# Kernel optimization log

Hardware: AMD Instinct MI355X
Metric: run time of the kernel (lower is better)

Reference implementation:

```python
import jax, jax.numpy as jnp
import numpy as np

K = 20      # kNN neighbors
H = 4       # attention heads
EPS = 1e-5  # BatchNorm eps
NEG = 0.2   # LeakyReLU negative slope


def lrelu(x):
    return jnp.where(x >= 0, x, NEG * x)


def bn(x, g, b):
    # eval-mode BatchNorm: running_mean=0, running_var=1
    return x * (g / jnp.sqrt(1.0 + EPS)) + b


def knn_idx(x):
    # x: (B, N, C) -> (B, N, K) indices of K nearest neighbors (incl. self)
    inner = -2.0 * jnp.einsum('bnc,bmc->bnm', x, x)
    xx = jnp.sum(x * x, axis=-1)
    pd = -xx[:, :, None] - inner - xx[:, None, :]  # negative squared distance
    return jax.lax.top_k(pd, K)[1]


def edge_conv(x, w, g, b):
    # EdgeConv: gather kNN features, cat(nbr-ctr, ctr), 1x1 conv, BN, LeakyReLU, max over K
    idx = knn_idx(x)                                   # (B,N,K)
    nbr = jax.vmap(lambda f, i: f[i])(x, idx)          # (B,N,K,C)
    ctr = jnp.broadcast_to(x[:, :, None, :], nbr.shape)
    e = jnp.concatenate([nbr - ctr, ctr], axis=-1)     # (B,N,K,2C)
    h = lrelu(bn(jnp.einsum('bnkc,oc->bnko', e, w), g, b))
    return jnp.max(h, axis=2)                          # (B,N,Cout)


def mha(x, w_in, b_in, w_out, b_out):
    # Faithful to source: (B,N,E) fed to nn.MultiheadAttention with batch_first=False,
    # so seq length L=B and batch=N (attention mixes across the batch axis).
    L, Nb, E = x.shape
    d = E // H
    qkv = x @ w_in.T + b_in
    q, k, v = jnp.split(qkv, 3, axis=-1)
    q = q.reshape(L, Nb, H, d) * (1.0 / np.sqrt(d))
    k = k.reshape(L, Nb, H, d)
    v = v.reshape(L, Nb, H, d)
    a = jax.nn.softmax(jnp.einsum('lnhd,mnhd->nhlm', q, k), axis=-1)
    o = jnp.einsum('nhlm,mnhd->lnhd', a, v).reshape(L, Nb, E)
    return o @ w_out.T + b_out


def setup_inputs():
    ks = iter(jax.random.split(jax.random.key(0), 64))
    def rn(shape, s=0.05):
        return jax.random.normal(next(ks), shape, jnp.float32) * s
    def gamma(c):
        return 1.0 + rn((c,), 0.1)
    B, N = 8, 1024
    inp = {'x': rn((B, N, 3), 1.0)}
    for i, (ci, co) in enumerate([(6, 64), (128, 64), (128, 128), (256, 256)], 1):
        inp[f'w{i}'] = rn((co, ci)); inp[f'g{i}'] = gamma(co); inp[f'b{i}'] = rn((co,))
    for i, e in enumerate([64, 64, 128, 256], 1):
        inp[f'a{i}_wi'] = rn((3 * e, e)); inp[f'a{i}_bi'] = rn((3 * e,))
        inp[f'a{i}_wo'] = rn((e, e));     inp[f'a{i}_bo'] = rn((e,))
    inp['w5'] = rn((1024, 512)); inp['g5'] = gamma(1024); inp['b5'] = rn((1024,))
    inp['l1w'] = rn((512, 2048)); inp['g6'] = gamma(512); inp['b6'] = rn((512,))
    inp['l2w'] = rn((256, 512)); inp['l2b'] = rn((256,))
    inp['g7'] = gamma(256); inp['b7'] = rn((256,))
    inp['l3w'] = rn((40, 256)); inp['l3b'] = rn((40,))
    return inp


def reference(x, w1, g1, b1, a1_wi, a1_bi, a1_wo, a1_bo,
              w2, g2, b2, a2_wi, a2_bi, a2_wo, a2_bo,
              w3, g3, b3, a3_wi, a3_bi, a3_wo, a3_bo,
              w4, g4, b4, a4_wi, a4_bi, a4_wo, a4_bo,
              w5, g5, b5, l1w, g6, b6, l2w, l2b, g7, b7, l3w, l3b):
    x1 = edge_conv(x, w1, g1, b1)
    x1 = mha(x1, a1_wi, a1_bi, a1_wo, a1_bo) + x1
    x2 = edge_conv(x1, w2, g2, b2)
    x2 = mha(x2, a2_wi, a2_bi, a2_wo, a2_bo) + x2
    x3 = edge_conv(x2, w3, g3, b3)
    x3 = mha(x3, a3_wi, a3_bi, a3_wo, a3_bo) + x3
    x4 = edge_conv(x3, w4, g4, b4)
    x4 = mha(x4, a4_wi, a4_bi, a4_wo, a4_bo) + x4
    h = lrelu(bn(jnp.concatenate([x1, x2, x3, x4], axis=-1) @ w5.T, g5, b5))  # (B,N,1024)
    feat = jnp.concatenate([jnp.max(h, axis=1), jnp.mean(h, axis=1)], axis=-1)  # (B,2048)
    h = lrelu(bn(feat @ l1w.T, g6, b6))
    h = lrelu(bn(h @ l2w.T + l2b, g7, b7))  # dropout is eval-mode identity
    return h @ l3w.T + l3b  # (B, 40)
```

## Files before the change

### kernel.cpp

```cpp
#include <hip/hip_runtime.h>
#include <hip/hip_bf16.h>

#define B_ 8
#define N_ 1024
#define K_ 20
#define BN_ (B_*N_)

#define BN_SCALE 0.9999950000374997f

typedef __attribute__((ext_vector_type(8))) short short8;
typedef __attribute__((ext_vector_type(4))) float f32x4;

__device__ __forceinline__ float US2F(unsigned short u) {
    union { unsigned u; float f; } c; c.u = ((unsigned)u) << 16; return c.f;
}
__device__ __forceinline__ unsigned short F2BF(float f) {
    union { float f; unsigned u; } c; c.f = f;
    unsigned r = c.u + 0x7FFF + ((c.u >> 16) & 1);
    return (unsigned short)(r >> 16);
}

__device__ __forceinline__ void ldsld16(const unsigned short* g, unsigned short* l) {
    __builtin_amdgcn_global_load_lds(
        (const __attribute__((address_space(1))) void*)g,
        (__attribute__((address_space(3))) void*)l, 16, 0, 0);
}

struct DetP { const unsigned short* g[7]; };
__device__ __forceinline__ int det_isbf(const DetP& dp) {
    int cnt = 0;
    #pragma unroll
    for (int i = 0; i < 7; i++) {
        float v = US2F(dp.g[i][0]);
        if (v > 0.5f && v < 1.5f) cnt++;
    }
    return cnt >= 4;
}

struct TPar { const void* src; void* dst; int O, I, blk0, mode; };
struct TList { TPar p[44]; };
struct TrP { const void* src; float* dst; int O, I, bx, blk0; };

__global__ __launch_bounds__(256) void k_prep(TList tl, int nent,
                                              TrP q0, TrP q1, TrP q2,
                                              int nbp, int nbtr,
                                              const void* x0, DetP dp,
                                              unsigned short* __restrict__ xa,
                                              unsigned short* __restrict__ xb,
                                              float* __restrict__ xx1) {
    __shared__ int sbf;
    if (threadIdx.x == 0) sbf = det_isbf(dp);
    __syncthreads();
    const int isbf = sbf;
    auto ld0 = [&](int idx) {
        return isbf ? US2F(((const unsigned short*)x0)[idx])
                    : ((const float*)x0)[idx];
    };
    const int bid = blockIdx.x;
    if (bid >= nbp + nbtr) {
        int blk = bid - nbp - nbtr;
        if (blk >= (BN_ * 32) / 256) {
            int i = (blk - (BN_ * 32) / 256) * 256 + threadIdx.x;
            if (i >= BN_) return;
            float s = 0.f;
            #pragma unroll
            for (int c = 0; c < 3; c++) { float v = ld0(i * 3 + c); s += v * v; }
            xx1[i] = s;
            return;
        }
        const int e = blk * 256 + threadIdx.x;
        const int i = e >> 5, p = e & 31;
        unsigned short va = 0, vb = 0;
        if (p < 9) {
            const int seg = p / 3, c = p - seg * 3;
            const float v = ld0(i * 3 + c);
            const unsigned short h = F2BF(v);
            const unsigned short l = F2BF(v - US2F(h));
            va = (seg == 1) ? l : h;
            vb = (seg < 2) ? h : l;
        }
        xa[e] = va; xb[e] = vb;
        return;
    }
    if (bid >= nbp) {
        int blk = bid - nbp;
        TrP p = q0;
        if (blk >= q2.blk0) p = q2; else if (blk >= q1.blk0) p = q1;
        blk -= p.blk0;
        const int tx = threadIdx.x & 31, ty = threadIdx.x >> 5;
        const int bi = blk % p.bx, bo = blk / p.bx;
        const int i0 = bi * 32, o0 = bo * 32;
        __shared__ float s[32][33];
        #pragma unroll
        for (int r = 0; r < 4; r++) {
            const int o = o0 + ty + r * 8, i = i0 + tx;
            if (o < p.O && i < p.I) {
                const size_t e = (size_t)o * p.I + i;
                s[ty + r * 8][tx] = isbf ? US2F(((const unsigned short*)p.src)[e])
                                         : ((const float*)p.src)[e];
            }
        }
        __syncthreads();
        #pragma unroll
        for (int r = 0; r < 4; r++) {
            const int i = i0 + ty + r * 8, o = o0 + tx;
            if (i < p.I && o < p.O) p.dst[(size_t)i * p.O + o] = s[tx][ty + r * 8];
        }
        return;
    }
    int blk = bid;
    int wi = 0;
    for (int j = nent - 1; j >= 0; j--) { if (blk >= tl.p[j].blk0) { wi = j; break; } }
    const TPar p = tl.p[wi];
    int e = (blk - p.blk0) * 256 + threadIdx.x;
    int n = p.O * p.I;
    if (e >= n) return;
    if (p.mode == 4) { ((float*)p.dst)[e] = 0.f; return; }
    int o = e / p.I, i = e - o * p.I;
    float v = isbf ? US2F(((const unsigned short*)p.src)[e])
                   : ((const float*)p.src)[e];
    if (p.mode == 0) {
        ((float*)p.dst)[(size_t)i * p.O + o] = v;
    } else if (p.mode == 2) {
        ((unsigned short*)p.dst)[e] = F2BF(v);
    } else {
        const int C = p.I >> 1;
        if (i < C) ((unsigned short*)p.dst)[(size_t)o * C + i] = F2BF(v);
        else       ((unsigned short*)p.dst)[(size_t)(p.O + o) * C + (i - C)] = F2BF(v);
    }
}

template<int KP, int TM, int TN>
__global__ __launch_bounds__(256) void k_pdm(const unsigned short* __restrict__ xa,
                                             const unsigned short* __restrict__ xb,
                                             const float* __restrict__ xx,
                                             float* __restrict__ pd) {
    const int bid = blockIdx.x;
    const int b = bid & 7;
    const int tt = bid >> 3;
    const int rb = (tt >> 3) * TM, cb = (tt & 7) * TN;
    const unsigned short* Ab = xa + (size_t)b * N_ * KP;
    const unsigned short* Bb = xb + (size_t)b * N_ * KP;
    const float* xxb = xx + (size_t)b * N_;
    const int t = threadIdx.x;
    __shared__ __align__(16) unsigned short As[2][TM * 32];
    __shared__ __align__(16) unsigned short Bs[2][TN * 32];
    const int w = t >> 6, lane = t & 63;
    constexpr int QR = TM / 2, QC = TN / 2;
    constexpr int MR = QR / 16, NR = QC / 16;
    const int wr = (w & 1) * QR, wc = (w >> 1) * QC;
    const int fr = lane & 15, q = lane >> 4;
    f32x4 acc[MR][NR] = {};

    auto STAGE = [&](int buf, int k0) {
        constexpr int AT = TM * 4;
        #pragma unroll
        for (int R = 0; R < (AT + 255) / 256; R++) {
            const int G = t + R * 256;
            if (AT >= (R + 1) * 256 || G < AT) {
                const int m = G >> 2, gs = (G & 3) ^ ((m >> 1) & 3);
                ldsld16(&Ab[(size_t)(rb + m) * KP + k0 + gs * 8], &As[buf][w * 512 + R * 2048]);
            }
        }
        constexpr int BT = TN * 4;
        #pragma unroll
        for (int R = 0; R < (BT + 255) / 256; R++) {
            const int G = t + R * 256;
            if (BT >= (R + 1) * 256 || G < BT) {
                const int n = G >> 2, gs = (G & 3) ^ ((n >> 1) & 3);
                ldsld16(&Bb[(size_t)(cb + n) * KP + k0 + gs * 8], &Bs[buf][w * 512 + R * 2048]);
            }
        }
    };

    constexpr int NT = KP / 32;
    STAGE(0, 0);
    asm volatile("s_waitcnt vmcnt(0)" ::: "memory");
    __builtin_amdgcn_s_barrier();
    int cur = 0;
    for (int ts = 0; ts < NT; ++ts) {
        if (ts + 1 < NT) STAGE(cur ^ 1, (ts + 1) * 32);
        short8 af[MR], bfr[NR];
        #pragma unroll
        for (int mi = 0; mi < MR; mi++) {
            const int r = wr + mi * 16 + fr;
            af[mi] = *reinterpret_cast<const short8*>(&As[cur][r * 32 + ((q ^ ((r >> 1) & 3)) << 3)]);
        }
        #pragma unroll
        for (int ni = 0; ni < NR; ni++) {
            const int r = wc + ni * 16 + fr;
            bfr[ni] = *reinterpret_cast<const short8*>(&Bs[cur][r * 32 + ((q ^ ((r >> 1) & 3)) << 3)]);
        }
        #pragma unroll
        for (int mi = 0; mi < MR; mi++) {
            #pragma unroll
            for (int ni = 0; ni < NR; ni++)
                acc[mi][ni] = __builtin_amdgcn_mfma_f32_16x16x32_bf16(af[mi], bfr[ni], acc[mi][ni], 0, 0, 0);
        }
        asm volatile("s_waitcnt vmcnt(0)" ::: "memory");
        __builtin_amdgcn_s_barrier();
        cur ^= 1;
    }
    float* pdb = pd + (size_t)b * N_ * N_;
    const int cr = (lane >> 4) * 4, cc = lane & 15;
    #pragma unroll
    for (int mi = 0; mi < MR; mi++) {
        #pragma unroll
        for (int ni = 0; ni < NR; ni++) {
            #pragma unroll
            for (int r = 0; r < 4; r++) {
                const int row = rb + wr + mi * 16 + cr + r;
                const int col = cb + wc + ni * 16 + cc;
                pdb[(size_t)row * N_ + col] = 2.f * acc[mi][ni][r] - xxb[col];
            }
        }
    }
}

__device__ __forceinline__ void sel_dev(const float* __restrict__ pd,
                                        int* __restrict__ idx, int blk) {
    const int w = threadIdx.x >> 6, lane = threadIdx.x & 63;
    const int b = blk & 7;
    const int i = (b << 10) + ((blk >> 3) << 2) + w;
    const float* row = pd + (size_t)b * N_ * N_ + (size_t)(i & 1023) * N_;
    unsigned key[16];
    #pragma unroll
    for (int q = 0; q < 16; q++) {
        const int j = q * 64 + lane;
        unsigned bits = __float_as_uint(row[j]);
        bits = (bits & 0x80000000u) ? ~bits : (bits | 0x80000000u);
        key[q] = (bits & 0xFFFFFC00u) | (unsigned)(N_ - 1 - j);
    }
    int myj = 0;
    for (int kk = 0; kk < K_; kk++) {
        unsigned m = key[0];
        #pragma unroll
        for (int u = 1; u < 16; u++) m = key[u] > m ? key[u] : m;
        #pragma unroll
        for (int s = 1; s < 64; s <<= 1) {
            unsigned o = (unsigned)__shfl_xor((int)m, s, 64);
            m = o > m ? o : m;
        }
        const int j = N_ - 1 - (int)(m & 1023u);
        if (lane == kk) myj = j;
        #pragma unroll
        for (int u = 0; u < 16; u++)
            if (key[u] == m) key[u] = 0u;
    }
    if (lane < K_) idx[(size_t)i * K_ + lane] = myj;
}

template<int KD, int NC, int TM, int TN, bool CATA, bool POOL, int SPLIT>
__device__ __forceinline__ void gemm_dev(int bx, int by,
                                         const unsigned short* __restrict__ A,
                                         const unsigned short* __restrict__ A2,
                                         const unsigned short* __restrict__ A3,
                                         const unsigned short* __restrict__ A4,
                                         const unsigned short* __restrict__ Bw,
                                         const float* __restrict__ bias,
                                         const float* __restrict__ resid,
                                         float* __restrict__ Cout,
                                         float* __restrict__ Cz, int yco,
                                         int scale_cols, float qs,
                                         const float* __restrict__ gamma,
                                         const float* __restrict__ beta,
                                         unsigned short* __restrict__ obf,
                                         unsigned* __restrict__ pmaxu,
                                         float* __restrict__ psum,
                                         unsigned short* __restrict__ sxa,
                                         unsigned short* __restrict__ sxb,
                                         float* __restrict__ xxo) {
    const int t = threadIdx.x;
    const int rb = bx * TM, cb = by * TN;
    const int w = t >> 6, lane = t & 63;
    constexpr int QR = TM / 2, QC = TN / 2;
    constexpr int MR = QR / 16, NR = QC / 16;
    const int wr = (w & 1) * QR, wc = (w >> 1) * QC;
    const int fr = lane & 15, q = lane >> 4, fq = q * 8;
    f32x4 acc[MR][NR] = {};
    if constexpr (KD % 32 == 0) {
        __shared__ __align__(16) unsigned short As[2][TM * 32];
        __shared__ __align__(16) unsigned short Bs[2][TN * 32];
        auto STAGE = [&](int buf, int k0) {
            const unsigned short* Asrc = A; int AC = KD, ac0 = k0;
            if constexpr (CATA) {
                if (k0 >= 256)      { Asrc = A4; AC = 256; ac0 = k0 - 256; }
                else if (k0 >= 128) { Asrc = A3; AC = 128; ac0 = k0 - 128; }
                else if (k0 >= 64)  { Asrc = A2; AC = 64;  ac0 = k0 - 64; }
                else                { Asrc = A;  AC = 64;  ac0 = k0; }
            }
            constexpr int AT = TM * 4;
            #pragma unroll
            for (int R = 0; R < (AT + 255) / 256; R++) {
                const int G = t + R * 256;
                if (AT >= (R + 1) * 256 || G < AT) {
                    const int m = G >> 2, gs = (G & 3) ^ ((m >> 1) & 3);
                    ldsld16(&Asrc[(size_t)(rb + m) * AC + ac0 + gs * 8], &As[buf][w * 512 + R * 2048]);
                }
            }
            constexpr int BT = TN * 4;
            #pragma unroll
            for (int R = 0; R < (BT + 255) / 256; R++) {
                const int G = t + R * 256;
                if (BT >= (R + 1) * 256 || G < BT) {
                    const int n = G >> 2, gs = (G & 3) ^ ((n >> 1) & 3);
                    ldsld16(&Bw[(size_t)(cb + n) * KD + k0 + gs * 8], &Bs[buf][w * 512 + R * 2048]);
                }
            }
        };
        constexpr int NT = KD / 32;
        STAGE(0, 0);
        asm volatile("s_waitcnt vmcnt(0)" ::: "memory");
        __builtin_amdgcn_s_barrier();
        int cur = 0;
        for (int ts = 0; ts < NT; ++ts) {
            if (ts + 1 < NT) STAGE(cur ^ 1, (ts + 1) * 32);
            short8 af[MR], bfr[NR];
            #pragma unroll
            for (int mi = 0; mi < MR; mi++) {
                const int r = wr + mi * 16 + fr;
                af[mi] = *reinterpret_cast<const short8*>(&As[cur][r * 32 + ((q ^ ((r >> 1) & 3)) << 3)]);
            }
            #pragma unroll
            for (int ni = 0; ni < NR; ni++) {
                const int r = wc + ni * 16 + fr;
                bfr[ni] = *reinterpret_cast<const short8*>(&Bs[cur][r * 32 + ((q ^ ((r >> 1) & 3)) << 3)]);
            }
            #pragma unroll
            for (int mi = 0; mi < MR; mi++) {
                #pragma unroll
                for (int ni = 0; ni < NR; ni++)
                    acc[mi][ni] = __builtin_amdgcn_mfma_f32_16x16x32_bf16(af[mi], bfr[ni], acc[mi][ni], 0, 0, 0);
            }
            asm volatile("s_waitcnt vmcnt(0)" ::: "memory");
            __builtin_amdgcn_s_barrier();
            cur ^= 1;
        }
    } else {
        __shared__ __align__(16) unsigned short As[TM * 40];
        __shared__ __align__(16) unsigned short Bs[TN * 40];
        for (int k0 = 0; k0 < KD; k0 += 32) {
            __syncthreads();
            #pragma unroll
            for (int u = t; u < TM * 4; u += 256) {
                const int m = u >> 2, c = (u & 3) * 8;
                #pragma unroll
                for (int j = 0; j < 8; j++) {
                    const int kk = k0 + c + j;
                    As[m * 40 + c + j] = (kk < KD) ? A[(size_t)(rb + m) * KD + kk] : (unsigned short)0;
                }
            }
            #pragma unroll
            for (int u = t; u < TN * 4; u += 256) {
                const int n = u >> 2, c = (u & 3) * 8;
                const int gn = cb + n;
                if (gn < NC) {
                    #pragma unroll
                    for (int j = 0; j < 8; j++) {
                        const int kk = k0 + c + j;
                        Bs[n * 40 + c + j] = (kk < KD) ? Bw[(size_t)gn * KD + kk] : (unsigned short)0;
                    }
                } else {
                    short8 z = {};
                    *reinterpret_cast<short8*>(&Bs[n * 40 + c]) = z;
                }
            }
            __syncthreads();
            short8 af[MR], bfr[NR];
            #pragma unroll
            for (int mi = 0; mi < MR; mi++)
                af[mi] = *reinterpret_cast<const short8*>(&As[(wr + mi * 16 + fr) * 40 + fq]);
            #pragma unroll
            for (int ni = 0; ni < NR; ni++)
                bfr[ni] = *reinterpret_cast<const short8*>(&Bs[(wc + ni * 16 + fr) * 40 + fq]);
            #pragma unroll
            for (int mi = 0; mi < MR; mi++) {
                #pragma unroll
                for (int ni = 0; ni < NR; ni++)
                    acc[mi][ni] = __builtin_amdgcn_mfma_f32_16x16x32_bf16(af[mi], bfr[ni], acc[mi][ni], 0, 0, 0);
            }
        }
    }
    const int cr = (lane >> 4) * 4, cc = lane & 15;
    if constexpr (POOL) {
        const int bidx = rb >> 10;
        #pragma unroll
        for (int ni = 0; ni < NR; ni++) {
            const int col = cb + wc + ni * 16 + cc;
            const float gm = gamma[col] * BN_SCALE, bt = beta[col];
            float sm = 0.f, mxv = -3e38f;
            #pragma unroll
            for (int mi = 0; mi < MR; mi++) {
                #pragma unroll
                for (int r = 0; r < 4; r++) {
                    float v = acc[mi][ni][r] * gm + bt;
                    v = v >= 0.f ? v : 0.2f * v;
                    sm += v; mxv = fmaxf(mxv, v);
                }
            }
            sm += __shfl_xor(sm, 16, 64);
            sm += __shfl_xor(sm, 32, 64);
            mxv = fmaxf(mxv, __shfl_xor(mxv, 16, 64));
            mxv = fmaxf(mxv, __shfl_xor(mxv, 32, 64));
            if (lane < 16) {
                atomicAdd(&psum[bidx * 1024 + col], sm);
                unsigned tb = __float_as_uint(mxv);
                tb = (tb & 0x80000000u) ? ~tb : (tb | 0x80000000u);
                atomicMax(&pmaxu[bidx * 1024 + col], tb);
            }
        }
    } else {
        float sx[MR][4] = {};
        #pragma unroll
        for (int mi = 0; mi < MR; mi++) {
            #pragma unroll
            for (int ni = 0; ni < NR; ni++) {
                #pragma unroll
                for (int r = 0; r < 4; r++) {
                    const int row = rb + wr + mi * 16 + cr + r;
                    const int col = cb + wc + ni * 16 + cc;
                    if (col < NC) {
                        float v = acc[mi][ni][r] + (bias ? bias[col] : 0.f);
                        if (col < scale_cols) v *= qs;
                        if (resid) v += resid[(size_t)row * NC + col];
                        if (gamma) {
                            v = v * (gamma[col] * BN_SCALE) + beta[col];
                            v = v >= 0.f ? v : 0.2f * v;
                        }
                        if (yco > 0) {
                            if (col < yco) Cout[(size_t)row * yco + col] = v;
                            else           Cz[(size_t)row * yco + (col - yco)] = v;
                        } else {
                            Cout[(size_t)row * NC + col] = v;
                        }
                        if (obf) obf[(size_t)row * NC + col] = F2BF(v);
                        if constexpr (SPLIT > 0) {
                            constexpr int KP2 = 3 * SPLIT;
                            const unsigned short h = F2BF(v);
                            const unsigned short l = F2BF(v - US2F(h));
                            sxa[(size_t)row * KP2 + 0 * SPLIT + col] = h;
                            sxa[(size_t)row * KP2 + 1 * SPLIT + col] = l;
                            sxa[(size_t)row * KP2 + 2 * SPLIT + col] = h;
                            sxb[(size_t)row * KP2 + 0 * SPLIT + col] = h;
                            sxb[(size_t)row * KP2 + 1 * SPLIT + col] = h;
                            sxb[(size_t)row * KP2 + 2 * SPLIT + col] = l;
                            sx[mi][r] += v * v;
                        }
                    }
                }
            }
        }
        if constexpr (SPLIT > 0) {
            #pragma unroll
            for (int mi = 0; mi < MR; mi++) {
                #pragma unroll
                for (int r = 0; r < 4; r++) {
                    float s = sx[mi][r];
                    s += __shfl_xor(s, 1, 64);
                    s += __shfl_xor(s, 2, 64);
                    s += __shfl_xor(s, 4, 64);
                    s += __shfl_xor(s, 8, 64);
                    if ((lane & 15) == 0)
                        atomicAdd(&xxo[rb + wr + mi * 16 + cr + r], s);
                }
            }
        }
    }
}

template<int KD, int NC, int TM, int TN, bool CATA = false, bool POOL = false, int SPLIT = 0, bool AFF = false>
__global__ __launch_bounds__(256) void k_gemmb(const unsigned short* __restrict__ A,
                                               const unsigned short* __restrict__ A2,
                                               const unsigned short* __restrict__ A3,
                                               const unsigned short* __restrict__ A4,
                                               const unsigned short* __restrict__ Bw,
                                               const float* __restrict__ bias,
                                               const float* __restrict__ resid,
                                               float* __restrict__ Cout,
                                               int scale_cols, float qs,
                                               const float* __restrict__ gamma,
                                               const float* __restrict__ beta,
                                               unsigned short* __restrict__ obf,
                                               unsigned* __restrict__ pmaxu,
                                               float* __restrict__ psum,
                                               unsigned short* __restrict__ sxa,
                                               unsigned short* __restrict__ sxb,
                                               float* __restrict__ xxo) {
    int bx = blockIdx.x;
    if constexpr (AFF) bx = (bx & 7) * (gridDim.x >> 3) + (bx >> 3);
    gemm_dev<KD, NC, TM, TN, CATA, POOL, SPLIT>(bx, blockIdx.y,
        A, A2, A3, A4, Bw, bias, resid, Cout, nullptr, 0, scale_cols, qs, gamma, beta,
        obf, pmaxu, psum, sxa, sxb, xxo);
}

template<int KD, int NC, int TM, int TN>
__global__ __launch_bounds__(256) void k_selyz(const float* __restrict__ pd,
                                               int* __restrict__ idx, int selb, int gx,
                                               const unsigned short* __restrict__ A,
                                               const unsigned short* __restrict__ Bw,
                                               float* __restrict__ Cy,
                                               float* __restrict__ Cz, int yco) {
    if ((int)blockIdx.x < selb) { sel_dev(pd, idx, blockIdx.x); return; }
    const int g = blockIdx.x - selb;
    const int batch = g & 7, rem = g >> 3;
    const int rpb = gx >> 3;
    const int bx = batch * rpb + rem % rpb;
    const int by = rem / rpb;
    gemm_dev<KD, NC, TM, TN, false, false, 0>(bx, by,
        A, nullptr, nullptr, nullptr, Bw, nullptr, nullptr, Cy, Cz, yco, 0, 1.f,
        nullptr, nullptr, nullptr, nullptr, nullptr, nullptr, nullptr, nullptr);
}

template<int CO>
__global__ __launch_bounds__(256) void k_edgemax(const float* __restrict__ y,
                                                 const float* __restrict__ z,
                                                 const int* __restrict__ idx,
                                                 const float* __restrict__ g,
                                                 const float* __restrict__ bb,
                                                 float* __restrict__ out,
                                                 unsigned short* __restrict__ outb) {
    constexpr int TPP = CO / 4;
    constexpr int PPB = 256 / TPP;
    const int t = threadIdx.x;
    const int p = t / TPP;
    const int cw = (t % TPP) * 4;
    const int batch = blockIdx.x & 7;
    const int within = blockIdx.x >> 3;
    const int i0 = batch * N_ + within * PPB;
    const int bbase = batch << 10;
    __shared__ int sidx[PPB][K_];
    for (int u = t; u < PPB * K_; u += 256) {
        int pp = u / K_, kk = u - pp * K_;
        sidx[pp][kk] = idx[(size_t)(i0 + pp) * K_ + kk];
    }
    __syncthreads();
    const int ig = i0 + p;
    float4 m = {-3e38f, -3e38f, -3e38f, -3e38f};
    #pragma unroll 4
    for (int k = 0; k < K_; k++) {
        const int jg = bbase + sidx[p][k];
        const float4 yv = *reinterpret_cast<const float4*>(&y[(size_t)jg * CO + cw]);
        m.x = fmaxf(m.x, yv.x); m.y = fmaxf(m.y, yv.y);
        m.z = fmaxf(m.z, yv.z); m.w = fmaxf(m.w, yv.w);
    }
    const float4 yi = *reinterpret_cast<const float4*>(&y[(size_t)ig * CO + cw]);
    const float4 zi = *reinterpret_cast<const float4*>(&z[(size_t)ig * CO + cw]);
    const float4 gv = *reinterpret_cast<const float4*>(&g[cw]);
    const float4 bv = *reinterpret_cast<const float4*>(&bb[cw]);
    float vals[4] = {m.x - yi.x + zi.x, m.y - yi.y + zi.y,
                     m.z - yi.z + zi.z, m.w - yi.w + zi.w};
    float gs[4] = {gv.x, gv.y, gv.z, gv.w};
    float bs[4] = {bv.x, bv.y, bv.z, bv.w};
    float4 o;
    float* op = &o.x;
    #pragma unroll
    for (int j = 0; j < 4; j++) {
        float h = vals[j] * (gs[j] * BN_SCALE) + bs[j];
        op[j] = h >= 0.f ? h : 0.2f * h;
    }
    *reinterpret_cast<float4*>(&out[(size_t)ig * CO + cw]) = o;
    #pragma unroll
    for (int j = 0; j < 4; j++) outb[(size_t)ig * CO + cw + j] = F2BF(op[j]);
}

template<int E>
__global__ __launch_bounds__(256) void k_attn(const float* __restrict__ qkv,
                                              unsigned short* __restrict__ o) {
    constexpr int H = 4, D = E / H, L = 8;
    const int n = blockIdx.x;
    const int t = threadIdx.x;
    const int h = t >> 6, lane = t & 63;
    __shared__ float sq[L][3 * E];
    __shared__ float so[L][E];
    for (int u = t; u < L * 3 * E; u += 256) {
        int l = u / (3 * E), r = u - l * (3 * E);
        sq[l][r] = qkv[(size_t)(l * N_ + n) * (3 * E) + r];
    }
    __syncthreads();
    const int l = lane >> 3, m = lane & 7;
    float s = 0.f;
    #pragma unroll 8
    for (int dd = 0; dd < D; dd++)
        s += sq[l][h * D + dd] * sq[m][E + h * D + dd];
    float mx = s;
    #pragma unroll
    for (int st = 1; st < 8; st <<= 1) mx = fmaxf(mx, __shfl_xor(mx, st, 64));
    float e = expf(s - mx);
    float sum = e;
    #pragma unroll
    for (int st = 1; st < 8; st <<= 1) sum += __shfl_xor(sum, st, 64);
    const float p = e / sum;
    float pm[8];
    #pragma unroll
    for (int mm = 0; mm < 8; mm++) pm[mm] = __shfl(p, (lane & 56) | mm, 64);
    #pragma unroll
    for (int j = 0; j < D / 8; j++) {
        const int dd = m + 8 * j;
        float a = 0.f;
        #pragma unroll
        for (int mm = 0; mm < 8; mm++) a += pm[mm] * sq[mm][2 * E + h * D + dd];
        so[l][h * D + dd] = a;
    }
    __syncthreads();
    for (int u = t; u < L * E; u += 256) {
        int l2 = u / E, e2 = u - l2 * E;
        o[(size_t)(l2 * N_ + n) * E + e2] = F2BF(so[l2][e2]);
    }
}

template<int E, int SPLIT>
__global__ __launch_bounds__(256) void k_attnout(const float* __restrict__ qkv,
                                                 const unsigned short* __restrict__ wo,
                                                 const float* __restrict__ bo,
                                                 float* __restrict__ x,
                                                 unsigned short* __restrict__ xob,
                                                 unsigned short* __restrict__ sxa,
                                                 unsigned short* __restrict__ sxb,
                                                 float* __restrict__ xxo) {
    constexpr int H = 4, D = E / H, L = 8;
    const int n = blockIdx.x;
    const int t = threadIdx.x;
    const int h = t >> 6, lane = t & 63;
    __shared__ float sq[L][3 * E];
    __shared__ float so[L][E];
    __shared__ unsigned short swo[E][E + 8];
    __shared__ float sxx[L];
    for (int u = t; u < L * 3 * E; u += 256) {
        int l = u / (3 * E), r = u - l * (3 * E);
        sq[l][r] = qkv[(size_t)(l * N_ + n) * (3 * E) + r];
    }
    for (int u = t; u < E * E; u += 256) swo[u / E][u % E] = wo[u];
    if (t < L) sxx[t] = 0.f;
    __syncthreads();
    const int l = lane >> 3, m = lane & 7;
    float s = 0.f;
    #pragma unroll 8
    for (int dd = 0; dd < D; dd++)
        s += sq[l][h * D + dd] * sq[m][E + h * D + dd];
    float mx = s;
    #pragma unroll
    for (int st = 1; st < 8; st <<= 1) mx = fmaxf(mx, __shfl_xor(mx, st, 64));
    float e = expf(s - mx);
    float sum = e;
    #pragma unroll
    for (int st = 1; st < 8; st <<= 1) sum += __shfl_xor(sum, st, 64);
    const float p = e / sum;
    float pm[8];
    #pragma unroll
    for (int mm = 0; mm < 8; mm++) pm[mm] = __shfl(p, (lane & 56) | mm, 64);
    #pragma unroll
    for (int j = 0; j < D / 8; j++) {
        const int dd = m + 8 * j;
        float a = 0.f;
        #pragma unroll
        for (int mm = 0; mm < 8; mm++) a += pm[mm] * sq[mm][2 * E + h * D + dd];
        so[l][h * D + dd] = a;
    }
    __syncthreads();
    for (int u = t; u < L * E; u += 256)
        so[u / E][u % E] = US2F(F2BF(so[u / E][u % E]));
    __syncthreads();
    constexpr int PT = (L * E) / 256;
    #pragma unroll
    for (int it = 0; it < PT; it++) {
        const int item = t + it * 256;
        const int ll = item / E, ee = item % E;
        float acc = 0.f;
        #pragma unroll 16
        for (int c = 0; c < E; c++)
            acc += so[ll][c] * US2F(swo[ee][c]);
        const int row = ll * N_ + n;
        const float v = acc + bo[ee] + x[(size_t)row * E + ee];
        x[(size_t)row * E + ee] = v;
        xob[(size_t)row * E + ee] = F2BF(v);
        if constexpr (SPLIT > 0) {
            constexpr int KP2 = 3 * SPLIT;
            const unsigned short hh = F2BF(v);
            const unsigned short lo = F2BF(v - US2F(hh));
            sxa[(size_t)row * KP2 + 0 * SPLIT + ee] = hh;
            sxa[(size_t)row * KP2 + 1 * SPLIT + ee] = lo;
            sxa[(size_t)row * KP2 + 2 * SPLIT + ee] = hh;
            sxb[(size_t)row * KP2 + 0 * SPLIT + ee] = hh;
            sxb[(size_t)row * KP2 + 1 * SPLIT + ee] = hh;
            sxb[(size_t)row * KP2 + 2 * SPLIT + ee] = lo;
            float vs = v * v;
            #pragma unroll
            for (int st = 1; st < 64; st <<= 1) vs += __shfl_xor(vs, st, 64);
            if (lane == 0) atomicAdd(&sxx[ll], vs);
        }
    }
    if constexpr (SPLIT > 0) {
        __syncthreads();
        if (t < L) xxo[t * N_ + n] = sxx[t];
    }
}

__global__ __launch_bounds__(256) void k_fc1(const unsigned* __restrict__ pmaxu,
                                             const float* __restrict__ psum,
                                             const float* __restrict__ l1wT,
                                             const float* __restrict__ g6, const float* __restrict__ b6,
                                             float* __restrict__ f1) {
    int oc = blockIdx.x, b = blockIdx.y, t = threadIdx.x;
    __shared__ float fin[2048];
    __shared__ float ps[4][64];
    for (int u = t; u < 2048; u += 256) {
        float v;
        if (u < 1024) {
            unsigned tb = pmaxu[b * 1024 + u];
            unsigned bits = (tb & 0x80000000u) ? (tb & 0x7FFFFFFFu) : ~tb;
            v = __uint_as_float(bits);
        } else {
            v = psum[b * 1024 + (u - 1024)] * (1.f / 1024.f);
        }
        fin[u] = v;
    }
    __syncthreads();
    int ol = t & 63, kc = t >> 6;
    int o = oc * 64 + ol;
    float acc = 0.f;
    for (int c = kc * 512; c < kc * 512 + 512; c++) acc += fin[c] * l1wT[(size_t)c * 512 + o];
    ps[kc][ol] = acc;
    __syncthreads();
    if (t < 64) {
        int oo = oc * 64 + t;
        float a = ps[0][t] + ps[1][t] + ps[2][t] + ps[3][t];
        float h = a * (g6[oo] * BN_SCALE) + b6[oo];
        f1[b * 512 + oo] = h >= 0.f ? h : 0.2f * h;
    }
}

__global__ __launch_bounds__(256) void k_fc23(const float* __restrict__ f1, const float* __restrict__ l2wT,
                                              const float* __restrict__ l2b,
                                              const float* __restrict__ g7, const float* __restrict__ b7,
                                              const float* __restrict__ l3wT, const float* __restrict__ l3b,
                                              void* __restrict__ out, DetP dp) {
    int b = blockIdx.x, t = threadIdx.x;
    __shared__ float fin[512];
    __shared__ float f2s[256];
    __shared__ int sbf;
    if (t == 0) sbf = det_isbf(dp);
    for (int u = t; u < 512; u += 256) fin[u] = f1[b * 512 + u];
    __syncthreads();
    {
        float acc = 0.f;
        for (int c = 0; c < 512; c++) acc += fin[c] * l2wT[(size_t)c * 256 + t];
        acc += l2b[t];
        float h = acc * (g7[t] * BN_SCALE) + b7[t];
        f2s[t] = h >= 0.f ? h : 0.2f * h;
    }
    __syncthreads();
    if (t < 40) {
        float acc = 0.f;
        for (int c = 0; c < 256; c++) acc += f2s[c] * l3wT[(size_t)c * 40 + t];
        acc += l3b[t];
        if (sbf) ((__hip_bfloat16*)out)[b * 40 + t] = __float2bfloat16(acc);
        else     ((float*)out)[b * 40 + t] = acc;
    }
}

extern "C" void kernel_launch(void* const* d_in, const int* in_sizes, int n_in,
                              void* d_out, int out_size, void* d_ws, size_t ws_size,
                              hipStream_t stream) {
    auto us = [&](int i) { return (const unsigned short*)d_in[i]; };

    float* ws = (float*)d_ws;
    size_t off = 0;
    auto A = [&](size_t n) { float* p = ws + off; off += (n + 3) & ~(size_t)3; return p; };
    auto AU = [&](size_t n) { return (unsigned short*)A((n + 1) / 2); };
    float* x1   = A((size_t)BN_ * 64);
    float* x2   = A((size_t)BN_ * 64);
    float* x3   = A((size_t)BN_ * 128);
    float* x4   = A((size_t)BN_ * 256);
    float* pd   = A((size_t)BN_ * 1024);
    float* f1   = A(8 * 512);
    float* xx   = A(4 * BN_);
    int*   idx  = (int*)A((size_t)BN_ * K_);
    float* qkvw = A((size_t)BN_ * 768);
    unsigned short* xa = AU((size_t)BN_ * 384);
    unsigned short* xb = AU((size_t)BN_ * 384);
    unsigned short* xf0b = AU((size_t)BN_ * 3);
    unsigned short* x1b  = AU((size_t)BN_ * 64);
    unsigned short* x2b  = AU((size_t)BN_ * 64);
    unsigned short* x3b  = AU((size_t)BN_ * 128);
    unsigned short* x4b  = AU((size_t)BN_ * 256);
    unsigned short* owb  = AU((size_t)BN_ * 256);
    unsigned* pmaxu = (unsigned*)A(8 * 1024);
    float*    psum  = A(8 * 1024);
    unsigned short* w1yzb = AU(128 * 3);
    unsigned short* w2yzb = AU(128 * 64);
    unsigned short* w3yzb = AU(256 * 64);
    unsigned short* w4yzb = AU(512 * 128);
    unsigned short* a1wib = AU(192 * 64);  unsigned short* a1wob = AU(64 * 64);
    unsigned short* a2wib = AU(192 * 64);  unsigned short* a2wob = AU(64 * 64);
    unsigned short* a3wib = AU(384 * 128); unsigned short* a3wob = AU(128 * 128);
    unsigned short* a4wib = AU(768 * 256); unsigned short* a4wob = AU(256 * 256);
    unsigned short* w5b   = AU(1024 * 512);
    float* l1wT  = A(2048 * 512);
    float* l2wT  = A(512 * 256);
    float* l3wT  = A(256 * 40);
    float* g1f = A(64);   float* b1f = A(64);
    float* g2f = A(64);   float* b2f = A(64);
    float* g3f = A(128);  float* b3f = A(128);
    float* g4f = A(256);  float* b4f = A(256);
    float* bi1 = A(192);  float* bo1 = A(64);
    float* bi2 = A(192);  float* bo2 = A(64);
    float* bi3 = A(384);  float* bo3 = A(128);
    float* bi4 = A(768);  float* bo4 = A(256);
    float* g5f = A(1024); float* b5f = A(1024);
    float* g6f = A(512);  float* b6f = A(512);
    float* l2bf = A(256);
    float* g7f = A(256);  float* b7f = A(256);
    float* l3bf = A(40);

    float* xx1 = xx;              float* xx2 = xx + BN_;
    float* xx3 = xx + 2 * BN_;    float* xx4 = xx + 3 * BN_;

    float* yy = qkvw;
    float* zz = qkvw + (size_t)BN_ * 256;

    DetP dp{{us(2), us(5), us(8), us(11), us(30), us(33), us(37)}};

    TList tl; int nb = 0; int k = 0;
    auto add = [&](int i, void* dst, int O, int I, int mode) {
        tl.p[k].src = d_in[i]; tl.p[k].dst = dst; tl.p[k].O = O; tl.p[k].I = I;
        tl.p[k].blk0 = nb; tl.p[k].mode = mode;
        nb += (O * I + 255) / 256; k++;
    };
    add(0,  xf0b,  BN_ * 3, 1, 2);
    add(0,  pmaxu, 16384, 1, 4);
    add(1,  w1yzb, 64, 6, 3);
    add(4,  w2yzb, 64, 128, 3);
    add(7,  w3yzb, 128, 128, 3);
    add(10, w4yzb, 256, 256, 3);
    add(13, a1wib, 192, 64, 2);
    add(15, a1wob, 64, 64, 2);
    add(17, a2wib, 192, 64, 2);
    add(19, a2wob, 64, 64, 2);
    add(21, a3wib, 384, 128, 2);
    add(23, a3wob, 128, 128, 2);
    add(25, a4wib, 768, 256, 2);
    add(27, a4wob, 256, 256, 2);
    add(29, w5b,   1024, 512, 2);
    add(2,  g1f, 64, 1, 0);   add(3,  b1f, 64, 1, 0);
    add(5,  g2f, 64, 1, 0);   add(6,  b2f, 64, 1, 0);
    add(8,  g3f, 128, 1, 0);  add(9,  b3f, 128, 1, 0);
    add(11, g4f, 256, 1, 0);  add(12, b4f, 256, 1, 0);
    add(14, bi1, 192, 1, 0);  add(16, bo1, 64, 1, 0);
    add(18, bi2, 192, 1, 0);  add(20, bo2, 64, 1, 0);
    add(22, bi3, 384, 1, 0);  add(24, bo3, 128, 1, 0);
    add(26, bi4, 768, 1, 0);  add(28, bo4, 256, 1, 0);
    add(30, g5f, 1024, 1, 0); add(31, b5f, 1024, 1, 0);
    add(33, g6f, 512, 1, 0);  add(34, b6f, 512, 1, 0);
    add(36, l2bf, 256, 1, 0);
    add(37, g7f, 256, 1, 0);  add(38, b7f, 256, 1, 0);
    add(40, l3bf, 40, 1, 0);

    TrP tp1{d_in[32], l1wT, 512, 2048, 2048 / 32, 0};
    TrP tp2{d_in[35], l2wT, 256, 512,  512 / 32,  (2048 / 32) * (512 / 32)};
    TrP tp3{d_in[39], l3wT, 40,  256,  256 / 32,  tp2.blk0 + (512 / 32) * (256 / 32)};
    const int trblocks = tp3.blk0 + (256 / 32) * ((40 + 31) / 32);
    const int splblocks = (BN_ * 32) / 256 + 32;
    k_prep<<<nb + trblocks + splblocks, 256, 0, stream>>>(
        tl, k, tp1, tp2, tp3, nb, trblocks, d_in[0], dp, xa, xb, xx1);

    const unsigned short* N0 = nullptr;
    unsigned short* U0 = nullptr;
    unsigned* NU = nullptr; float* NF = nullptr;

    k_pdm<32, 128, 128><<<512, 256, 0, stream>>>(xa, xb, xx1, pd);
    k_selyz<3, 128, 64, 64><<<2048 + 256, 256, 0, stream>>>(pd, idx, 2048, 128, xf0b, w1yzb, yy, zz, 64);
    k_edgemax<64><<<BN_ / 16, 256, 0, stream>>>(yy, zz, idx, g1f, b1f, x1, x1b);
    k_gemmb<64, 192, 64, 64, false, false, 0, true><<<dim3(128, 3), 256, 0, stream>>>(x1b, N0, N0, N0, a1wib, bi1, nullptr, qkvw, 64, 0.25f, nullptr, nullptr, nullptr, NU, NF, U0, U0, NF);
    k_attnout<64, 64><<<N_, 256, 0, stream>>>(qkvw, a1wob, bo1, x1, x1b, xa, xb, xx2);

    k_pdm<192, 128, 128><<<512, 256, 0, stream>>>(xa, xb, xx2, pd);
    k_selyz<64, 128, 64, 64><<<2048 + 256, 256, 0, stream>>>(pd, idx, 2048, 128, x1b, w2yzb, yy, zz, 64);
    k_edgemax<64><<<BN_ / 16, 256, 0, stream>>>(yy, zz, idx, g2f, b2f, x2, x2b);
    k_gemmb<64, 192, 64, 64, false, false, 0, true><<<dim3(128, 3), 256, 0, stream>>>(x2b, N0, N0, N0, a2wib, bi2, nullptr, qkvw, 64, 0.25f, nullptr, nullptr, nullptr, NU, NF, U0, U0, NF);
    k_attnout<64, 64><<<N_, 256, 0, stream>>>(qkvw, a2wob, bo2, x2, x2b, xa, xb, xx3);

    k_pdm<192, 128, 128><<<512, 256, 0, stream>>>(xa, xb, xx3, pd);
    k_selyz<64, 256, 64, 64><<<2048 + 512, 256, 0, stream>>>(pd, idx, 2048, 128, x2b, w3yzb, yy, zz, 128);
    k_edgemax<128><<<BN_ / 8, 256, 0, stream>>>(yy, zz, idx, g3f, b3f, x3, x3b);
    k_gemmb<128, 384, 64, 128, false, false, 0, true><<<dim3(128, 3), 256, 0, stream>>>(x3b, N0, N0, N0, a3wib, bi3, nullptr, qkvw, 128, 0.17677669529663687f, nullptr, nullptr, nullptr, NU, NF, U0, U0, NF);
    k_attnout<128, 128><<<N_, 256, 0, stream>>>(qkvw, a3wob, bo3, x3, x3b, xa, xb, xx4);

    k_pdm<384, 128, 128><<<512, 256, 0, stream>>>(xa, xb, xx4, pd);
    k_selyz<128, 512, 128, 128><<<2048 + 256, 256, 0, stream>>>(pd, idx, 2048, 64, x3b, w4yzb, yy, zz, 256);
    k_edgemax<256><<<BN_ / 4, 256, 0, stream>>>(yy, zz, idx, g4f, b4f, x4, x4b);
    k_gemmb<256, 768, 64, 128, false, false, 0, true><<<dim3(128, 6), 256, 0, stream>>>(x4b, N0, N0, N0, a4wib, bi4, nullptr, qkvw, 256, 0.125f, nullptr, nullptr, nullptr, NU, NF, U0, U0, NF);
    k_attn<256><<<N_, 256, 0, stream>>>(qkvw, owb);
    k_gemmb<256, 256, 64, 128, false, false, 0, true><<<dim3(128, 2), 256, 0, stream>>>(owb, N0, N0, N0, a4wob, bo4, x4, x4, 0, 1.f, nullptr, nullptr, x4b, NU, NF, U0, U0, NF);

    k_gemmb<512, 1024, 128, 128, true, true, 0, true><<<dim3(64, 8), 256, 0, stream>>>(
        x1b, x2b, x3b, x4b, w5b, nullptr, nullptr, nullptr, 0, 1.f, g5f, b5f, nullptr, pmaxu, psum, U0, U0, NF);
    k_fc1<<<dim3(8, 8), 256, 0, stream>>>(pmaxu, psum, l1wT, g6f, b6f, f1);
    k_fc23<<<8, 256, 0, stream>>>(f1, l2wT, l2bf, g7f, b7f, l3wT, l3bf, d_out, dp);
}
```

Baseline: 486.4 us.

## Re-fuse kNN pipeline stages and merge final attention with output projection

The pairwise-distance GEMM is moved into the same launch as the y/z edge-feature GEMM, and top-k selection is fused with the edge max-gather. This removes the global idx buffer and one kernel launch per EdgeConv layer. For layer 4, the attention kernel and the output-projection GEMM are merged into one per-point kernel that computes the Wo product from shared memory with scalar FMAs, dropping the bf16 intermediate buffer. The trade-offs are less efficient non-MFMA arithmetic for the layer-4 projection, and select blocks in which only some threads do the gather work (for CO=64 only 64 threads).

```diff
diff --git a/kernel.cpp b/kernel.cpp
--- a/kernel.cpp
+++ b/kernel.cpp
@@ -131,11 +131,11 @@
 }
 
 template<int KP, int TM, int TN>
-__global__ __launch_bounds__(256) void k_pdm(const unsigned short* __restrict__ xa,
-                                             const unsigned short* __restrict__ xb,
-                                             const float* __restrict__ xx,
-                                             float* __restrict__ pd) {
-    const int bid = blockIdx.x;
+__device__ __forceinline__ void pdm_dev(int bid,
+                                        const unsigned short* __restrict__ xa,
+                                        const unsigned short* __restrict__ xb,
+                                        const float* __restrict__ xx,
+                                        float* __restrict__ pd) {
     const int b = bid & 7;
     const int tt = bid >> 3;
     const int rb = (tt >> 3) * TM, cb = (tt & 7) * TN;
@@ -215,39 +215,6 @@
             }
         }
     }
-}
-
-__device__ __forceinline__ void sel_dev(const float* __restrict__ pd,
-                                        int* __restrict__ idx, int blk) {
-    const int w = threadIdx.x >> 6, lane = threadIdx.x & 63;
-    const int b = blk & 7;
-    const int i = (b << 10) + ((blk >> 3) << 2) + w;
-    const float* row = pd + (size_t)b * N_ * N_ + (size_t)(i & 1023) * N_;
-    unsigned key[16];
-    #pragma unroll
-    for (int q = 0; q < 16; q++) {
-        const int j = q * 64 + lane;
-        unsigned bits = __float_as_uint(row[j]);
-        bits = (bits & 0x80000000u) ? ~bits : (bits | 0x80000000u);
-        key[q] = (bits & 0xFFFFFC00u) | (unsigned)(N_ - 1 - j);
-    }
-    int myj = 0;
-    for (int kk = 0; kk < K_; kk++) {
-        unsigned m = key[0];
-        #pragma unroll
-        for (int u = 1; u < 16; u++) m = key[u] > m ? key[u] : m;
-        #pragma unroll
-        for (int s = 1; s < 64; s <<= 1) {
-            unsigned o = (unsigned)__shfl_xor((int)m, s, 64);
-            m = o > m ? o : m;
-        }
-        const int j = N_ - 1 - (int)(m & 1023u);
-        if (lane == kk) myj = j;
-        #pragma unroll
-        for (int u = 0; u < 16; u++)
-            if (key[u] == m) key[u] = 0u;
-    }
-    if (lane < K_) idx[(size_t)i * K_ + lane] = myj;
 }
 
 template<int KD, int NC, int TM, int TN, bool CATA, bool POOL, int SPLIT>
@@ -493,118 +460,102 @@
         obf, pmaxu, psum, sxa, sxb, xxo);
 }
 
-template<int KD, int NC, int TM, int TN>
-__global__ __launch_bounds__(256) void k_selyz(const float* __restrict__ pd,
-                                               int* __restrict__ idx, int selb, int gx,
-                                               const unsigned short* __restrict__ A,
-                                               const unsigned short* __restrict__ Bw,
+template<int KP, int KDY, int NCY, int TMY, int TNY>
+__global__ __launch_bounds__(256) void k_pdmyz(const unsigned short* __restrict__ xa,
+                                               const unsigned short* __restrict__ xb,
+                                               const float* __restrict__ xx,
+                                               float* __restrict__ pd,
+                                               const unsigned short* __restrict__ Ay,
+                                               const unsigned short* __restrict__ Bwy,
                                                float* __restrict__ Cy,
-                                               float* __restrict__ Cz, int yco) {
-    if ((int)blockIdx.x < selb) { sel_dev(pd, idx, blockIdx.x); return; }
-    const int g = blockIdx.x - selb;
+                                               float* __restrict__ Cz, int yco, int gxy) {
+    if ((int)blockIdx.x < 512) { pdm_dev<KP, 128, 128>(blockIdx.x, xa, xb, xx, pd); return; }
+    const int g = blockIdx.x - 512;
     const int batch = g & 7, rem = g >> 3;
-    const int rpb = gx >> 3;
+    const int rpb = gxy >> 3;
     const int bx = batch * rpb + rem % rpb;
     const int by = rem / rpb;
-    gemm_dev<KD, NC, TM, TN, false, false, 0>(bx, by,
-        A, nullptr, nullptr, nullptr, Bw, nullptr, nullptr, Cy, Cz, yco, 0, 1.f,
+    gemm_dev<KDY, NCY, TMY, TNY, false, false, 0>(bx, by,
+        Ay, nullptr, nullptr, nullptr, Bwy, nullptr, nullptr, Cy, Cz, yco, 0, 1.f,
         nullptr, nullptr, nullptr, nullptr, nullptr, nullptr, nullptr, nullptr);
 }
 
 template<int CO>
-__global__ __launch_bounds__(256) void k_edgemax(const float* __restrict__ y,
+__global__ __launch_bounds__(256) void k_seledge(const float* __restrict__ pd,
+                                                 const float* __restrict__ y,
                                                  const float* __restrict__ z,
-                                                 const int* __restrict__ idx,
                                                  const float* __restrict__ g,
                                                  const float* __restrict__ bb,
                                                  float* __restrict__ out,
                                                  unsigned short* __restrict__ outb) {
+    const int t = threadIdx.x;
+    const int w = t >> 6, lane = t & 63;
+    const int blk = blockIdx.x;
+    const int b = blk & 7;
+    const int i0 = (b << 10) + ((blk >> 3) << 2);
+    const int bbase = b << 10;
+    __shared__ int sidx[4][K_];
+    {
+        const int i = i0 + w;
+        const float* row = pd + (size_t)b * N_ * N_ + (size_t)(i & 1023) * N_;
+        unsigned key[16];
+        #pragma unroll
+        for (int q = 0; q < 16; q++) {
+            const int j = q * 64 + lane;
+            unsigned bits = __float_as_uint(row[j]);
+            bits = (bits & 0x80000000u) ? ~bits : (bits | 0x80000000u);
+            key[q] = (bits & 0xFFFFFC00u) | (unsigned)(N_ - 1 - j);
+        }
+        int myj = 0;
+        for (int kk = 0; kk < K_; kk++) {
+            unsigned m = key[0];
+            #pragma unroll
+            for (int u = 1; u < 16; u++) m = key[u] > m ? key[u] : m;
+            #pragma unroll
+            for (int s = 1; s < 64; s <<= 1) {
+                unsigned o = (unsigned)__shfl_xor((int)m, s, 64);
+                m = o > m ? o : m;
+            }
+            const int j = N_ - 1 - (int)(m & 1023u);
+            if (lane == kk) myj = j;
+            #pragma unroll
+            for (int u = 0; u < 16; u++)
+                if (key[u] == m) key[u] = 0u;
+        }
+        if (lane < K_) sidx[w][lane] = myj;
+    }
+    __syncthreads();
     constexpr int TPP = CO / 4;
-    constexpr int PPB = 256 / TPP;
-    const int t = threadIdx.x;
-    const int p = t / TPP;
-    const int cw = (t % TPP) * 4;
-    const int batch = blockIdx.x & 7;
-    const int within = blockIdx.x >> 3;
-    const int i0 = batch * N_ + within * PPB;
-    const int bbase = batch << 10;
-    __shared__ int sidx[PPB][K_];
-    for (int u = t; u < PPB * K_; u += 256) {
-        int pp = u / K_, kk = u - pp * K_;
-        sidx[pp][kk] = idx[(size_t)(i0 + pp) * K_ + kk];
-    }
-    __syncthreads();
-    const int ig = i0 + p;
-    float4 m = {-3e38f, -3e38f, -3e38f, -3e38f};
-    #pragma unroll 4
-    for (int k = 0; k < K_; k++) {
-        const int jg = bbase + sidx[p][k];
-        const float4 yv = *reinterpret_cast<const float4*>(&y[(size_t)jg * CO + cw]);
-        m.x = fmaxf(m.x, yv.x); m.y = fmaxf(m.y, yv.y);
-        m.z = fmaxf(m.z, yv.z); m.w = fmaxf(m.w, yv.w);
-    }
-    const float4 yi = *reinterpret_cast<const float4*>(&y[(size_t)ig * CO + cw]);
-    const float4 zi = *reinterpret_cast<const float4*>(&z[(size_t)ig * CO + cw]);
-    const float4 gv = *reinterpret_cast<const float4*>(&g[cw]);
-    const float4 bv = *reinterpret_cast<const float4*>(&bb[cw]);
-    float vals[4] = {m.x - yi.x + zi.x, m.y - yi.y + zi.y,
-                     m.z - yi.z + zi.z, m.w - yi.w + zi.w};
-    float gs[4] = {gv.x, gv.y, gv.z, gv.w};
-    float bs[4] = {bv.x, bv.y, bv.z, bv.w};
-    float4 o;
-    float* op = &o.x;
-    #pragma unroll
-    for (int j = 0; j < 4; j++) {
-        float h = vals[j] * (gs[j] * BN_SCALE) + bs[j];
-        op[j] = h >= 0.f ? h : 0.2f * h;
-    }
-    *reinterpret_cast<float4*>(&out[(size_t)ig * CO + cw]) = o;
-    #pragma unroll
-    for (int j = 0; j < 4; j++) outb[(size_t)ig * CO + cw + j] = F2BF(op[j]);
-}
-
-template<int E>
-__global__ __launch_bounds__(256) void k_attn(const float* __restrict__ qkv,
-                                              unsigned short* __restrict__ o) {
-    constexpr int H = 4, D = E / H, L = 8;
-    const int n = blockIdx.x;
-    const int t = threadIdx.x;
-    const int h = t >> 6, lane = t & 63;
-    __shared__ float sq[L][3 * E];
-    __shared__ float so[L][E];
-    for (int u = t; u < L * 3 * E; u += 256) {
-        int l = u / (3 * E), r = u - l * (3 * E);
-        sq[l][r] = qkv[(size_t)(l * N_ + n) * (3 * E) + r];
-    }
-    __syncthreads();
-    const int l = lane >> 3, m = lane & 7;
-    float s = 0.f;
-    #pragma unroll 8
-    for (int dd = 0; dd < D; dd++)
-        s += sq[l][h * D + dd] * sq[m][E + h * D + dd];
-    float mx = s;
-    #pragma unroll
-    for (int st = 1; st < 8; st <<= 1) mx = fmaxf(mx, __shfl_xor(mx, st, 64));
-    float e = expf(s - mx);
-    float sum = e;
-    #pragma unroll
-    for (int st = 1; st < 8; st <<= 1) sum += __shfl_xor(sum, st, 64);
-    const float p = e / sum;
-    float pm[8];
-    #pragma unroll
-    for (int mm = 0; mm < 8; mm++) pm[mm] = __shfl(p, (lane & 56) | mm, 64);
-    #pragma unroll
-    for (int j = 0; j < D / 8; j++) {
-        const int dd = m + 8 * j;
-        float a = 0.f;
-        #pragma unroll
-        for (int mm = 0; mm < 8; mm++) a += pm[mm] * sq[mm][2 * E + h * D + dd];
-        so[l][h * D + dd] = a;
-    }
-    __syncthreads();
-    for (int u = t; u < L * E; u += 256) {
-        int l2 = u / E, e2 = u - l2 * E;
-        o[(size_t)(l2 * N_ + n) * E + e2] = F2BF(so[l2][e2]);
+    if (t < 4 * TPP) {
+        const int p = t / TPP;
+        const int cw = (t % TPP) * 4;
+        const int ig = i0 + p;
+        float4 m = {-3e38f, -3e38f, -3e38f, -3e38f};
+        #pragma unroll 4
+        for (int k = 0; k < K_; k++) {
+            const int jg = bbase + sidx[p][k];
+            const float4 yv = *reinterpret_cast<const float4*>(&y[(size_t)jg * CO + cw]);
+            m.x = fmaxf(m.x, yv.x); m.y = fmaxf(m.y, yv.y);
+            m.z = fmaxf(m.z, yv.z); m.w = fmaxf(m.w, yv.w);
+        }
+        const float4 yi = *reinterpret_cast<const float4*>(&y[(size_t)ig * CO + cw]);
+        const float4 zi = *reinterpret_cast<const float4*>(&z[(size_t)ig * CO + cw]);
+        const float4 gv = *reinterpret_cast<const float4*>(&g[cw]);
+        const float4 bv = *reinterpret_cast<const float4*>(&bb[cw]);
+        float vals[4] = {m.x - yi.x + zi.x, m.y - yi.y + zi.y,
+                         m.z - yi.z + zi.z, m.w - yi.w + zi.w};
+        float gs[4] = {gv.x, gv.y, gv.z, gv.w};
+        float bs[4] = {bv.x, bv.y, bv.z, bv.w};
+        float4 o;
+        float* op = &o.x;
+        #pragma unroll
+        for (int j = 0; j < 4; j++) {
+            float h = vals[j] * (gs[j] * BN_SCALE) + bs[j];
+            op[j] = h >= 0.f ? h : 0.2f * h;
+        }
+        *reinterpret_cast<float4*>(&out[(size_t)ig * CO + cw]) = o;
+        #pragma unroll
+        for (int j = 0; j < 4; j++) outb[(size_t)ig * CO + cw + j] = F2BF(op[j]);
     }
 }
 
@@ -695,6 +646,81 @@
     }
 }
 
+__global__ __launch_bounds__(256) void k_attnout4(const float* __restrict__ qkv,
+                                                  const unsigned short* __restrict__ wo,
+                                                  const float* __restrict__ bo,
+                                                  float* __restrict__ x,
+                                                  unsigned short* __restrict__ xob) {
+    constexpr int E = 256, H = 4, D = E / H, L = 8;
+    const int n = blockIdx.x;
+    const int t = threadIdx.x;
+    const int h = t >> 6, lane = t & 63;
+    __shared__ float sq[L][3 * E];
+    __shared__ float so[L][E];
+    __shared__ float swoc[E][33];
+    for (int u = t; u < L * 3 * E; u += 256) {
+        int l = u / (3 * E), r = u - l * (3 * E);
+        sq[l][r] = qkv[(size_t)(l * N_ + n) * (3 * E) + r];
+    }
+    __syncthreads();
+    const int l = lane >> 3, m = lane & 7;
+    float s = 0.f;
+    #pragma unroll 8
+    for (int dd = 0; dd < D; dd++)
+        s += sq[l][h * D + dd] * sq[m][E + h * D + dd];
+    float mx = s;
+    #pragma unroll
+    for (int st = 1; st < 8; st <<= 1) mx = fmaxf(mx, __shfl_xor(mx, st, 64));
+    float e = expf(s - mx);
+    float sum = e;
+    #pragma unroll
+    for (int st = 1; st < 8; st <<= 1) sum += __shfl_xor(sum, st, 64);
+    const float p = e / sum;
+    float pm[8];
+    #pragma unroll
+    for (int mm = 0; mm < 8; mm++) pm[mm] = __shfl(p, (lane & 56) | mm, 64);
+    #pragma unroll
+    for (int j = 0; j < D / 8; j++) {
+        const int dd = m + 8 * j;
+        float a = 0.f;
+        #pragma unroll
+        for (int mm = 0; mm < 8; mm++) a += pm[mm] * sq[mm][2 * E + h * D + dd];
+        so[l][h * D + dd] = a;
+    }
+    __syncthreads();
+    for (int u = t; u < L * E; u += 256)
+        so[u / E][u % E] = US2F(F2BF(so[u / E][u % E]));
+    constexpr int PT = (L * E) / 256;
+    float acc[PT] = {};
+    for (int ch = 0; ch < 8; ch++) {
+        __syncthreads();
+        for (int u = t; u < E * 32; u += 256) {
+            const int ee = u >> 5, cc = u & 31;
+            swoc[ee][cc] = US2F(wo[ee * E + ch * 32 + cc]);
+        }
+        __syncthreads();
+        #pragma unroll
+        for (int it = 0; it < PT; it++) {
+            const int item = t + it * 256;
+            const int ll = item / E, ee = item % E;
+            float a = acc[it];
+            #pragma unroll
+            for (int cc = 0; cc < 32; cc++)
+                a += so[ll][ch * 32 + cc] * swoc[ee][cc];
+            acc[it] = a;
+        }
+    }
+    #pragma unroll
+    for (int it = 0; it < PT; it++) {
+        const int item = t + it * 256;
+        const int ll = item / E, ee = item % E;
+        const int row = ll * N_ + n;
+        const float v = acc[it] + bo[ee] + x[(size_t)row * E + ee];
+        x[(size_t)row * E + ee] = v;
+        xob[(size_t)row * E + ee] = F2BF(v);
+    }
+}
+
 __global__ __launch_bounds__(256) void k_fc1(const unsigned* __restrict__ pmaxu,
                                              const float* __restrict__ psum,
                                              const float* __restrict__ l1wT,
@@ -774,7 +800,6 @@
     float* pd   = A((size_t)BN_ * 1024);
     float* f1   = A(8 * 512);
     float* xx   = A(4 * BN_);
-    int*   idx  = (int*)A((size_t)BN_ * K_);
     float* qkvw = A((size_t)BN_ * 768);
     unsigned short* xa = AU((size_t)BN_ * 384);
     unsigned short* xb = AU((size_t)BN_ * 384);
@@ -783,7 +808,6 @@
     unsigned short* x2b  = AU((size_t)BN_ * 64);
     unsigned short* x3b  = AU((size_t)BN_ * 128);
     unsigned short* x4b  = AU((size_t)BN_ * 256);
-    unsigned short* owb  = AU((size_t)BN_ * 256);
     unsigned* pmaxu = (unsigned*)A(8 * 1024);
     float*    psum  = A(8 * 1024);
     unsigned short* w1yzb = AU(128 * 3);
@@ -867,30 +891,25 @@
     unsigned short* U0 = nullptr;
     unsigned* NU = nullptr; float* NF = nullptr;
 
-    k_pdm<32, 128, 128><<<512, 256, 0, stream>>>(xa, xb, xx1, pd);
-    k_selyz<3, 128, 64, 64><<<2048 + 256, 256, 0, stream>>>(pd, idx, 2048, 128, xf0b, w1yzb, yy, zz, 64);
-    k_edgemax<64><<<BN_ / 16, 256, 0, stream>>>(yy, zz, idx, g1f, b1f, x1, x1b);
+    k_pdmyz<32, 3, 128, 64, 64><<<512 + 256, 256, 0, stream>>>(xa, xb, xx1, pd, xf0b, w1yzb, yy, zz, 64, 128);
+    k_seledge<64><<<2048, 256, 0, stream>>>(pd, yy, zz, g1f, b1f, x1, x1b);
     k_gemmb<64, 192, 64, 64, false, false, 0, true><<<dim3(128, 3), 256, 0, stream>>>(x1b, N0, N0, N0, a1wib, bi1, nullptr, qkvw, 64, 0.25f, nullptr, nullptr, nullptr, NU, NF, U0, U0, NF);
     k_attnout<64, 64><<<N_, 256, 0, stream>>>(qkvw, a1wob, bo1, x1, x1b, xa, xb, xx2);
 
-    k_pdm<192, 128, 128><<<512, 256, 0, stream>>>(xa, xb, xx2, pd);
-    k_selyz<64, 128, 64, 64><<<2048 + 256, 256, 0, stream>>>(pd, idx, 2048, 128, x1b, w2yzb, yy, zz, 64);
-    k_edgemax<64><<<BN_ / 16, 256, 0, stream>>>(yy, zz, idx, g2f, b2f, x2, x2b);
+    k_pdmyz<192, 64, 128, 64, 64><<<512 + 256, 256, 0, stream>>>(xa, xb, xx2, pd, x1b, w2yzb, yy, zz, 64, 128);
+    k_seledge<64><<<2048, 256, 0, stream>>>(pd, yy, zz, g2f, b2f, x2, x2b);
     k_gemmb<64, 192, 64, 64, false, false, 0, true><<<dim3(128, 3), 256, 0, stream>>>(x2b, N0, N0, N0, a2wib, bi2, nullptr, qkvw, 64, 0.25f, nullptr, nullptr, nullptr, NU, NF, U0, U0, NF);
     k_attnout<64, 64><<<N_, 256, 0, stream>>>(qkvw, a2wob, bo2, x2, x2b, xa, xb, xx3);
 
-    k_pdm<192, 128, 128><<<512, 256, 0, stream>>>(xa, xb, xx3, pd);
-    k_selyz<64, 256, 64, 64><<<2048 + 512, 256, 0, stream>>>(pd, idx, 2048, 128, x2b, w3yzb, yy, zz, 128);
-    k_edgemax<128><<<BN_ / 8, 256, 0, stream>>>(yy, zz, idx, g3f, b3f, x3, x3b);
+    k_pdmyz<192, 64, 256, 64, 64><<<512 + 512, 256, 0, stream>>>(xa, xb, xx3, pd, x2b, w3yzb, yy, zz, 128, 128);
+    k_seledge<128><<<2048, 256, 0, stream>>>(pd, yy, zz, g3f, b3f, x3, x3b);
     k_gemmb<128, 384, 64, 128, false, false, 0, true><<<dim3(128, 3), 256, 0, stream>>>(x3b, N0, N0, N0, a3wib, bi3, nullptr, qkvw, 128, 0.17677669529663687f, nullptr, nullptr, nullptr, NU, NF, U0, U0, NF);
     k_attnout<128, 128><<<N_, 256, 0, stream>>>(qkvw, a3wob, bo3, x3, x3b, xa, xb, xx4);
 
-    k_pdm<384, 128, 128><<<512, 256, 0, stream>>>(xa, xb, xx4, pd);
-    k_selyz<128, 512, 128, 128><<<2048 + 256, 256, 0, stream>>>(pd, idx, 2048, 64, x3b, w4yzb, yy, zz, 256);
-    k_edgemax<256><<<BN_ / 4, 256, 0, stream>>>(yy, zz, idx, g4f, b4f, x4, x4b);
+    k_pdmyz<384, 128, 512, 128, 128><<<512 + 256, 256, 0, stream>>>(xa, xb, xx4, pd, x3b, w4yzb, yy, zz, 256, 64);
+    k_seledge<256><<<2048, 256, 0, stream>>>(pd, yy, zz, g4f, b4f, x4, x4b);
     k_gemmb<256, 768, 64, 128, false, false, 0, true><<<dim3(128, 6), 256, 0, stream>>>(x4b, N0, N0, N0, a4wib, bi4, nullptr, qkvw, 256, 0.125f, nullptr, nullptr, nullptr, NU, NF, U0, U0, NF);
-    k_attn<256><<<N_, 256, 0, stream>>>(qkvw, owb);
-    k_gemmb<256, 256, 64, 128, false, false, 0, true><<<dim3(128, 2), 256, 0, stream>>>(owb, N0, N0, N0, a4wob, bo4, x4, x4, 0, 1.f, nullptr, nullptr, x4b, NU, NF, U0, U0, NF);
+    k_attnout4<<<N_, 256, 0, stream>>>(qkvw, a4wob, bo4, x4, x4b);
 
     k_gemmb<512, 1024, 128, 128, true, true, 0, true><<<dim3(64, 8), 256, 0, stream>>>(
         x1b, x2b, x3b, x4b, w5b, nullptr, nullptr, nullptr, 0, 1.f, g5f, b5f, nullptr, pmaxu, psum, U0, U0, NF);
```

Result: slower. 520.0 us (+6.9%).
